# Kernel tuning notes

Hardware: AMD Instinct MI355X
Metric: run time of the kernel (lower is better)

Reference implementation:

```python
import jax, jax.numpy as jnp
import numpy as np

B, L, D = 4, 4096, 1024
H, W = 16, 64          # n_heads, window_size
HD = D // H            # head_dim
EPS = 1e-5


def setup_inputs() -> dict:
    key = jax.random.key(0)
    ks = jax.random.split(key, 3)
    s = 1.0 / np.sqrt(D)
    x = jax.random.normal(ks[0], (B, L, D), dtype=jnp.float32)
    Wqkv = (jax.random.normal(ks[1], (3 * D, D), dtype=jnp.float32) * s)
    bqkv = jnp.zeros((3 * D,), dtype=jnp.float32)
    Wproj = (jax.random.normal(ks[2], (D, D), dtype=jnp.float32) * s)
    bproj = jnp.zeros((D,), dtype=jnp.float32)
    gamma = jnp.ones((D,), dtype=jnp.float32)
    beta = jnp.zeros((D,), dtype=jnp.float32)
    return {"x": x, "Wqkv": Wqkv, "bqkv": bqkv, "Wproj": Wproj,
            "bproj": bproj, "gamma": gamma, "beta": beta}


def reference(x, Wqkv, bqkv, Wproj, bproj, gamma, beta):
    scale = HD ** -0.5
    nw = L // W  # L is a multiple of W, so pad_len == 0 (same math as padded path)
    # QKV projection -> [3, B, H, L, HD]
    qkv = (x @ Wqkv.T + bqkv).reshape(B, L, 3, H, HD).transpose(2, 0, 3, 1, 4)
    q, k, v = qkv[0], qkv[1], qkv[2]
    # split into non-overlapping windows: [B, H, nw, W, HD]
    q = q.reshape(B, H, nw, W, HD)
    k = k.reshape(B, H, nw, W, HD)
    v = v.reshape(B, H, nw, W, HD)
    attn = jax.nn.softmax(jnp.einsum('bhnqd,bhnkd->bhnqk', q, k) * scale, axis=-1)
    out = jnp.einsum('bhnqk,bhnkd->bhnqd', attn, v)  # dropout is identity in eval
    out = out.reshape(B, H, L, HD).transpose(0, 2, 1, 3).reshape(B, L, D)
    out = out @ Wproj.T + bproj
    y = out + x
    mean = jnp.mean(y, axis=-1, keepdims=True)
    var = jnp.mean((y - mean) ** 2, axis=-1, keepdims=True)
    return (y - mean) * jax.lax.rsqrt(var + EPS) * gamma + beta
```

## Files before the change

### kernel.cpp

```cpp
#include <hip/hip_runtime.h>
#include <stdint.h>


typedef __attribute__((ext_vector_type(8))) short short8;
typedef __attribute__((ext_vector_type(4))) float float4v;
typedef unsigned short us;

#define GAS const __attribute__((address_space(1))) void
#define LAS __attribute__((address_space(3))) void

__device__ __forceinline__ float bf2f(us u) {
  return __uint_as_float(((unsigned int)u) << 16);
}
__device__ __forceinline__ us f2bf(float f) {
  unsigned int u = __float_as_uint(f);
  unsigned int r = u + 0x7FFFu + ((u >> 16) & 1u);
  return (us)(r >> 16);
}
__device__ __forceinline__ int4 stage8(const float* p) {
  float4 a = *(const float4*)p;
  float4 b = *(const float4*)(p + 4);
  int4 r;
  us* u = (us*)&r;
  u[0] = f2bf(a.x); u[1] = f2bf(a.y); u[2] = f2bf(a.z); u[3] = f2bf(a.w);
  u[4] = f2bf(b.x); u[5] = f2bf(b.y); u[6] = f2bf(b.z); u[7] = f2bf(b.w);
  return r;
}
__device__ __forceinline__ int4 stage8(const us* p) { return *(const int4*)p; }
__device__ __forceinline__ void stc(us* p, float v) { *p = f2bf(v); }
__device__ __forceinline__ void stc(float* p, float v) { *p = v; }

__global__ __launch_bounds__(256) void cast_bf16(const float* __restrict__ src,
                                                 us* __restrict__ dst, int n8) {
  const int i = blockIdx.x * 256 + threadIdx.x;
  if (i < n8) *(int4*)(dst + (size_t)i * 8) = stage8(src + (size_t)i * 8);
}

template <int N, int K, int EPI, typename CT>
__global__ __launch_bounds__(256) void gemm_async(
    const us* __restrict__ A, const us* __restrict__ Bt,
    const float* __restrict__ bias, const float* __restrict__ resid,
    CT* __restrict__ C) {
  __shared__ __align__(16) us As[128 * 64];
  __shared__ __align__(16) us Bs[128 * 64];
  const int tid = threadIdx.x;
  const int lane = tid & 63;
  const int wave = tid >> 6;
  const int wm = wave >> 1, wn = wave & 1;
  const int lr = lane & 15, lq = lane >> 4;
  const int m0 = blockIdx.y * 128;
  const int n0 = blockIdx.x * 128;
  const int trow = tid >> 3;
  const int tcol = (((tid & 7) ^ (trow & 7)) * 8);

  float4v acc[4][4];
#pragma unroll
  for (int i = 0; i < 4; i++)
#pragma unroll
    for (int j = 0; j < 4; j++) acc[i][j] = (float4v)0.0f;

  for (int k0 = 0; k0 < K; k0 += 64) {
#pragma unroll
    for (int p = 0; p < 4; p++) {
      const us* ga = A + (size_t)(m0 + p * 32 + trow) * K + k0 + tcol;
      const us* gb = Bt + (size_t)(n0 + p * 32 + trow) * K + k0 + tcol;
      __builtin_amdgcn_global_load_lds((GAS*)ga, (LAS*)&As[(p * 256 + tid) * 8], 16, 0, 0);
      __builtin_amdgcn_global_load_lds((GAS*)gb, (LAS*)&Bs[(p * 256 + tid) * 8], 16, 0, 0);
    }
    __syncthreads();
#pragma unroll
    for (int kk8 = 0; kk8 < 2; kk8++) {
      short8 af[4], bfv[4];
#pragma unroll
      for (int mt = 0; mt < 4; mt++)
        af[mt] = *(const short8*)&As[(wm * 64 + mt * 16 + lr) * 64 +
                                     (((lq + kk8 * 4) ^ (lr & 7)) * 8)];
#pragma unroll
      for (int nt = 0; nt < 4; nt++)
        bfv[nt] = *(const short8*)&Bs[(wn * 64 + nt * 16 + lr) * 64 +
                                      (((lq + kk8 * 4) ^ (lr & 7)) * 8)];
#pragma unroll
      for (int mt = 0; mt < 4; mt++)
#pragma unroll
        for (int nt = 0; nt < 4; nt++)
          acc[mt][nt] = __builtin_amdgcn_mfma_f32_16x16x32_bf16(
              af[mt], bfv[nt], acc[mt][nt], 0, 0, 0);
    }
    __syncthreads();
  }

  float bb[4];
#pragma unroll
  for (int nt = 0; nt < 4; nt++) bb[nt] = bias[n0 + wn * 64 + nt * 16 + lr];
#pragma unroll
  for (int mt = 0; mt < 4; mt++) {
    const int rbase = m0 + wm * 64 + mt * 16 + lq * 4;
#pragma unroll
    for (int nt = 0; nt < 4; nt++) {
      const int col = n0 + wn * 64 + nt * 16 + lr;
#pragma unroll
      for (int r = 0; r < 4; r++) {
        float v = acc[mt][nt][r] + bb[nt];
        size_t idx = (size_t)(rbase + r) * N + col;
        if (EPI) v += resid[idx];
        stc(&C[idx], v);
      }
    }
  }
}

__global__ __launch_bounds__(256) void attn_mfma(
    const us* __restrict__ qkv, us* __restrict__ attn) {
  __shared__ __align__(16) us Vt[64 * 64];
  __shared__ __align__(16) us Pl[4 * 16 * 64];
  const int wid = blockIdx.x;
  const int wi = wid & 63;
  const int h = (wid >> 6) & 15;
  const int b = wid >> 10;
  const int tid = threadIdx.x;
  const int lane = tid & 63;
  const int w = tid >> 6;
  const int lr = lane & 15, lq = lane >> 4;
  const int rowbase = b * 4096 + wi * 64;

  {
    const int r = lane;
    const int cs = w * 16;
    const us* vsrc = qkv + (size_t)(rowbase + r) * 3072 + 2048 + h * 64 + cs;
    int4 v0 = *(const int4*)vsrc;
    int4 v1 = *(const int4*)(vsrc + 8);
    const us* vv0 = (const us*)&v0;
    const us* vv1 = (const us*)&v1;
#pragma unroll
    for (int i = 0; i < 8; i++) {
      const int d = cs + i;
      Vt[d * 64 + (((r >> 3) ^ (d & 7)) * 8) + (r & 7)] = vv0[i];
    }
#pragma unroll
    for (int i = 0; i < 8; i++) {
      const int d = cs + 8 + i;
      Vt[d * 64 + (((r >> 3) ^ (d & 7)) * 8) + (r & 7)] = vv1[i];
    }
  }

  short8 aq[2];
  {
    const us* qrow = qkv + (size_t)(rowbase + w * 16 + lr) * 3072 + h * 64 + lq * 8;
    aq[0] = *(const short8*)qrow;
    aq[1] = *(const short8*)(qrow + 32);
  }
  float4v s[4];
#pragma unroll
  for (int nt = 0; nt < 4; nt++) s[nt] = (float4v)0.0f;
#pragma unroll
  for (int kk8 = 0; kk8 < 2; kk8++) {
#pragma unroll
    for (int nt = 0; nt < 4; nt++) {
      const us* krow = qkv + (size_t)(rowbase + nt * 16 + lr) * 3072 + 1024 +
                       h * 64 + kk8 * 32 + lq * 8;
      short8 bk = *(const short8*)krow;
      s[nt] = __builtin_amdgcn_mfma_f32_16x16x32_bf16(aq[kk8], bk, s[nt], 0, 0, 0);
    }
  }

  float p[4][4];
#pragma unroll
  for (int r = 0; r < 4; r++) {
    float mx = -1e30f;
#pragma unroll
    for (int nt = 0; nt < 4; nt++) {
      s[nt][r] *= 0.125f;
      mx = fmaxf(mx, s[nt][r]);
    }
    mx = fmaxf(mx, __shfl_xor(mx, 1));
    mx = fmaxf(mx, __shfl_xor(mx, 2));
    mx = fmaxf(mx, __shfl_xor(mx, 4));
    mx = fmaxf(mx, __shfl_xor(mx, 8));
    float sum = 0.f;
#pragma unroll
    for (int nt = 0; nt < 4; nt++) {
      p[nt][r] = __expf(s[nt][r] - mx);
      sum += p[nt][r];
    }
    sum += __shfl_xor(sum, 1);
    sum += __shfl_xor(sum, 2);
    sum += __shfl_xor(sum, 4);
    sum += __shfl_xor(sum, 8);
    const float inv = 1.0f / sum;
#pragma unroll
    for (int nt = 0; nt < 4; nt++) p[nt][r] *= inv;
  }

  us* pw = Pl + w * 1024;
#pragma unroll
  for (int nt = 0; nt < 4; nt++) {
    const int c = nt * 16 + lr;
#pragma unroll
    for (int r = 0; r < 4; r++) {
      const int row = lq * 4 + r;
      pw[row * 64 + (((c >> 3) ^ (row & 7)) * 8) + (c & 7)] = f2bf(p[nt][r]);
    }
  }
  __syncthreads();

  float4v o[4];
#pragma unroll
  for (int nt = 0; nt < 4; nt++) o[nt] = (float4v)0.0f;
#pragma unroll
  for (int kk8 = 0; kk8 < 2; kk8++) {
    short8 pa = *(const short8*)&pw[lr * 64 + (((lq + kk8 * 4) ^ (lr & 7)) * 8)];
#pragma unroll
    for (int nt = 0; nt < 4; nt++) {
      const int d = nt * 16 + lr;
      short8 vb = *(const short8*)&Vt[d * 64 + (((lq + kk8 * 4) ^ (d & 7)) * 8)];
      o[nt] = __builtin_amdgcn_mfma_f32_16x16x32_bf16(pa, vb, o[nt], 0, 0, 0);
    }
  }

#pragma unroll
  for (int nt = 0; nt < 4; nt++) {
    const int d = nt * 16 + lr;
#pragma unroll
    for (int r = 0; r < 4; r++) {
      const int tok = rowbase + w * 16 + lq * 4 + r;
      attn[(size_t)tok * 1024 + h * 64 + d] = f2bf(o[nt][r]);
    }
  }
}

template <int N, int K, int EPI, typename AT, typename CT>
__global__ __launch_bounds__(256) void gemm_bt(
    const AT* __restrict__ A, const float* __restrict__ Bt,
    const float* __restrict__ bias, const float* __restrict__ resid,
    CT* __restrict__ C) {
  __shared__ __align__(16) us As[128 * 64];
  __shared__ __align__(16) us Bs[128 * 64];
  const int tid = threadIdx.x;
  const int lane = tid & 63;
  const int wave = tid >> 6;
  const int wm = wave >> 1, wn = wave & 1;
  const int lr = lane & 15, lq = lane >> 4;
  const int m0 = blockIdx.y * 128;
  const int n0 = blockIdx.x * 128;
  const int trow = tid >> 3;
  const int tcol = (tid & 7) * 8;

  float4v acc[4][4];
#pragma unroll
  for (int i = 0; i < 4; i++)
#pragma unroll
    for (int j = 0; j < 4; j++) acc[i][j] = (float4v)0.0f;

  for (int k0 = 0; k0 < K; k0 += 64) {
    int4 av[4], bv[4];
#pragma unroll
    for (int p = 0; p < 4; p++) {
      av[p] = stage8(A + (size_t)(m0 + p * 32 + trow) * K + k0 + tcol);
      bv[p] = stage8(Bt + (size_t)(n0 + p * 32 + trow) * K + k0 + tcol);
    }
#pragma unroll
    for (int p = 0; p < 4; p++) {
      *(int4*)&As[(p * 256 + tid) * 8] = av[p];
      *(int4*)&Bs[(p * 256 + tid) * 8] = bv[p];
    }
    __syncthreads();
#pragma unroll
    for (int kk = 0; kk < 64; kk += 32) {
      short8 af[4], bfv[4];
#pragma unroll
      for (int mt = 0; mt < 4; mt++)
        af[mt] = *(const short8*)&As[(wm * 64 + mt * 16 + lr) * 64 + kk + lq * 8];
#pragma unroll
      for (int nt = 0; nt < 4; nt++)
        bfv[nt] = *(const short8*)&Bs[(wn * 64 + nt * 16 + lr) * 64 + kk + lq * 8];
#pragma unroll
      for (int mt = 0; mt < 4; mt++)
#pragma unroll
        for (int nt = 0; nt < 4; nt++)
          acc[mt][nt] = __builtin_amdgcn_mfma_f32_16x16x32_bf16(
              af[mt], bfv[nt], acc[mt][nt], 0, 0, 0);
    }
    __syncthreads();
  }

  float bb[4];
#pragma unroll
  for (int nt = 0; nt < 4; nt++) bb[nt] = bias[n0 + wn * 64 + nt * 16 + lr];
#pragma unroll
  for (int mt = 0; mt < 4; mt++) {
    const int rbase = m0 + wm * 64 + mt * 16 + lq * 4;
#pragma unroll
    for (int nt = 0; nt < 4; nt++) {
      const int col = n0 + wn * 64 + nt * 16 + lr;
#pragma unroll
      for (int r = 0; r < 4; r++) {
        float v = acc[mt][nt][r] + bb[nt];
        size_t idx = (size_t)(rbase + r) * N + col;
        if (EPI) v += resid[idx];
        stc(&C[idx], v);
      }
    }
  }
}

__global__ __launch_bounds__(256) void attn_win(
    const us* __restrict__ qkv, us* __restrict__ attn) {
  __shared__ float qs[64][65];
  __shared__ float ks[64][65];
  __shared__ float vs[64][65];
  const int wid = blockIdx.x;
  const int wi = wid & 63;
  const int h = (wid >> 6) & 15;
  const int b = wid >> 10;
  const int t = threadIdx.x;
  const int rowbase = b * 4096 + wi * 64;
  {
    const int r = t >> 2;
    const int cs = (t & 3) * 16;
    const us* base = qkv + (size_t)(rowbase + r) * 3072 + h * 64 + cs;
#pragma unroll
    for (int s = 0; s < 3; s++) {
      float* dst = (s == 0) ? &qs[r][cs] : (s == 1) ? &ks[r][cs] : &vs[r][cs];
      const us* src = base + s * 1024;
#pragma unroll
      for (int half = 0; half < 2; half++) {
        int4 dv = *(const int4*)(src + half * 8);
        const us* tp = (const us*)&dv;
#pragma unroll
        for (int i = 0; i < 8; i++) dst[half * 8 + i] = bf2f(tp[i]);
      }
    }
  }
  __syncthreads();
  const int r0 = (t >> 4) * 4;
  const int c0 = (t & 15) * 4;
  float acc[4][4] = {};
#pragma unroll 8
  for (int k = 0; k < 64; k++) {
    float qv[4], kv[4];
#pragma unroll
    for (int i = 0; i < 4; i++) qv[i] = qs[r0 + i][k];
#pragma unroll
    for (int j = 0; j < 4; j++) kv[j] = ks[c0 + j][k];
#pragma unroll
    for (int i = 0; i < 4; i++)
#pragma unroll
      for (int j = 0; j < 4; j++) acc[i][j] += qv[i] * kv[j];
  }
  __syncthreads();
#pragma unroll
  for (int i = 0; i < 4; i++)
#pragma unroll
    for (int j = 0; j < 4; j++) qs[r0 + i][c0 + j] = acc[i][j] * 0.125f;
  __syncthreads();
  {
    const int rr = t >> 2;
    const int cs = (t & 3) * 16;
    float pv[16];
    float m = -1e30f;
#pragma unroll
    for (int i = 0; i < 16; i++) {
      pv[i] = qs[rr][cs + i];
      m = fmaxf(m, pv[i]);
    }
    m = fmaxf(m, __shfl_xor(m, 1));
    m = fmaxf(m, __shfl_xor(m, 2));
    float ssum = 0.f;
#pragma unroll
    for (int i = 0; i < 16; i++) {
      pv[i] = __expf(pv[i] - m);
      ssum += pv[i];
    }
    ssum += __shfl_xor(ssum, 1);
    ssum += __shfl_xor(ssum, 2);
    const float inv = 1.0f / ssum;
#pragma unroll
    for (int i = 0; i < 16; i++) qs[rr][cs + i] = pv[i] * inv;
  }
  __syncthreads();
  float o[4][4] = {};
#pragma unroll 8
  for (int k = 0; k < 64; k++) {
    float pr[4], vv[4];
#pragma unroll
    for (int i = 0; i < 4; i++) pr[i] = qs[r0 + i][k];
#pragma unroll
    for (int j = 0; j < 4; j++) vv[j] = vs[k][c0 + j];
#pragma unroll
    for (int i = 0; i < 4; i++)
#pragma unroll
      for (int j = 0; j < 4; j++) o[i][j] += pr[i] * vv[j];
  }
#pragma unroll
  for (int i = 0; i < 4; i++)
#pragma unroll
    for (int j = 0; j < 4; j++)
      attn[(size_t)(rowbase + r0 + i) * 1024 + h * 64 + c0 + j] = f2bf(o[i][j]);
}

__global__ __launch_bounds__(256) void ln_inplace(
    float* __restrict__ y, const float* __restrict__ gamma,
    const float* __restrict__ beta) {
  const int row = blockIdx.x;
  const int t = threadIdx.x;
  float* yr = y + (size_t)row * 1024;
  float4 v = *(const float4*)(yr + t * 4);
  float s1 = v.x + v.y + v.z + v.w;
  float s2 = v.x * v.x + v.y * v.y + v.z * v.z + v.w * v.w;
#pragma unroll
  for (int off = 32; off > 0; off >>= 1) {
    s1 += __shfl_down(s1, off);
    s2 += __shfl_down(s2, off);
  }
  __shared__ float red[8];
  const int lane = t & 63, wave = t >> 6;
  if (lane == 0) {
    red[wave] = s1;
    red[4 + wave] = s2;
  }
  __syncthreads();
  if (t == 0) {
    red[0] = red[0] + red[1] + red[2] + red[3];
    red[4] = red[4] + red[5] + red[6] + red[7];
  }
  __syncthreads();
  const float mean = red[0] * (1.0f / 1024.0f);
  const float var = red[4] * (1.0f / 1024.0f) - mean * mean;
  const float rstd = rsqrtf(var + 1e-5f);
  float4 g = *(const float4*)(gamma + t * 4);
  float4 bt = *(const float4*)(beta + t * 4);
  float4 o;
  o.x = (v.x - mean) * rstd * g.x + bt.x;
  o.y = (v.y - mean) * rstd * g.y + bt.y;
  o.z = (v.z - mean) * rstd * g.z + bt.z;
  o.w = (v.w - mean) * rstd * g.w + bt.w;
  *(float4*)(yr + t * 4) = o;
}

extern "C" void kernel_launch(void* const* d_in, const int* in_sizes, int n_in,
                              void* d_out, int out_size, void* d_ws,
                              size_t ws_size, hipStream_t stream) {
  const float* x = (const float*)d_in[0];
  const float* Wqkv = (const float*)d_in[1];
  const float* bqkv = (const float*)d_in[2];
  const float* Wproj = (const float*)d_in[3];
  const float* bproj = (const float*)d_in[4];
  const float* gamma = (const float*)d_in[5];
  const float* beta = (const float*)d_in[6];
  float* out = (float*)d_out;

  us* qkv = (us*)d_ws;
  us* attn = qkv + (size_t)16384 * 3072;
  us* xb = attn + (size_t)16384 * 1024;
  us* Wqkvb = xb + (size_t)16384 * 1024;
  us* Wprojb = Wqkvb + (size_t)3072 * 1024;
  const size_t need =
      ((size_t)16384 * 3072 + 3 * (size_t)16384 * 1024 + (size_t)3072 * 1024 +
       (size_t)1024 * 1024) * sizeof(us);

  if (ws_size >= need) {
    cast_bf16<<<(16384 * 1024 / 8 + 255) / 256, 256, 0, stream>>>(x, xb,
                                                                  16384 * 128);
    cast_bf16<<<(3072 * 1024 / 8 + 255) / 256, 256, 0, stream>>>(Wqkv, Wqkvb,
                                                                 3072 * 128);
    cast_bf16<<<(1024 * 1024 / 8 + 255) / 256, 256, 0, stream>>>(Wproj, Wprojb,
                                                                 1024 * 128);
    gemm_async<3072, 1024, 0, us><<<dim3(24, 128), 256, 0, stream>>>(
        xb, Wqkvb, bqkv, nullptr, qkv);
    attn_mfma<<<4096, 256, 0, stream>>>(qkv, attn);
    gemm_async<1024, 1024, 1, float><<<dim3(8, 128), 256, 0, stream>>>(
        attn, Wprojb, bproj, x, out);
  } else {
    gemm_bt<3072, 1024, 0, float, us><<<dim3(24, 128), 256, 0, stream>>>(
        x, Wqkv, bqkv, nullptr, qkv);
    attn_win<<<4096, 256, 0, stream>>>(qkv, attn);
    gemm_bt<1024, 1024, 1, us, float><<<dim3(8, 128), 256, 0, stream>>>(
        attn, Wproj, bproj, x, out);
  }
  ln_inplace<<<16384, 256, 0, stream>>>(out, gamma, beta);
}
```

Measured before the change: 385.4 us.

## Use 256x256 double-buffered GEMM tiles with async LDS prefetch and priority hints

Replaces the 128x128 single-buffered bf16 GEMM with a 256x256 tile over 512 threads. The next K-tile is double-buffered via global_load_lds and a partial vmcnt wait, so loads overlap the MFMA work. Barriers around each MFMA cluster and s_setprio raise MFMA issue priority. The larger tile improves operand reuse but uses 128KB of LDS and more accumulator registers, and launches fewer blocks, which hurts occupancy and tail balance, especially for the 1024-wide projection (256 blocks).

```diff
diff --git a/kernel.cpp b/kernel.cpp
--- a/kernel.cpp
+++ b/kernel.cpp
@@ -37,76 +37,111 @@
 }
 
 template <int N, int K, int EPI, typename CT>
-__global__ __launch_bounds__(256) void gemm_async(
+__global__ __launch_bounds__(512, 1) void gemm256(
     const us* __restrict__ A, const us* __restrict__ Bt,
     const float* __restrict__ bias, const float* __restrict__ resid,
     CT* __restrict__ C) {
-  __shared__ __align__(16) us As[128 * 64];
-  __shared__ __align__(16) us Bs[128 * 64];
+  __shared__ __align__(16) us As[2][256 * 64];
+  __shared__ __align__(16) us Bs[2][256 * 64];
   const int tid = threadIdx.x;
   const int lane = tid & 63;
   const int wave = tid >> 6;
-  const int wm = wave >> 1, wn = wave & 1;
+  const int wm = wave >> 2;
+  const int wn = wave & 3;
   const int lr = lane & 15, lq = lane >> 4;
-  const int m0 = blockIdx.y * 128;
-  const int n0 = blockIdx.x * 128;
+  const int m0 = blockIdx.y * 256;
+  const int n0 = blockIdx.x * 256;
   const int trow = tid >> 3;
   const int tcol = (((tid & 7) ^ (trow & 7)) * 8);
 
-  float4v acc[4][4];
-#pragma unroll
-  for (int i = 0; i < 4; i++)
+  constexpr int NT = K / 64;
+
+  float4v acc[8][4];
+#pragma unroll
+  for (int i = 0; i < 8; i++)
 #pragma unroll
     for (int j = 0; j < 4; j++) acc[i][j] = (float4v)0.0f;
 
-  for (int k0 = 0; k0 < K; k0 += 64) {
-#pragma unroll
-    for (int p = 0; p < 4; p++) {
-      const us* ga = A + (size_t)(m0 + p * 32 + trow) * K + k0 + tcol;
-      const us* gb = Bt + (size_t)(n0 + p * 32 + trow) * K + k0 + tcol;
-      __builtin_amdgcn_global_load_lds((GAS*)ga, (LAS*)&As[(p * 256 + tid) * 8], 16, 0, 0);
-      __builtin_amdgcn_global_load_lds((GAS*)gb, (LAS*)&Bs[(p * 256 + tid) * 8], 16, 0, 0);
-    }
-    __syncthreads();
+#define STAGE256(buf, t)                                                       \
+  do {                                                                         \
+    const size_t kof = (size_t)(t) * 64;                                       \
+    _Pragma("unroll") for (int q = 0; q < 4; q++) {                            \
+      const us* ga = A + (size_t)(m0 + q * 64 + trow) * K + kof + tcol;        \
+      __builtin_amdgcn_global_load_lds((GAS*)ga,                               \
+          (LAS*)&As[buf][(q * 512 + tid) * 8], 16, 0, 0);                      \
+    }                                                                          \
+    _Pragma("unroll") for (int q = 0; q < 4; q++) {                            \
+      const us* gb = Bt + (size_t)(n0 + q * 64 + trow) * K + kof + tcol;       \
+      __builtin_amdgcn_global_load_lds((GAS*)gb,                               \
+          (LAS*)&Bs[buf][(q * 512 + tid) * 8], 16, 0, 0);                      \
+    }                                                                          \
+  } while (0)
+
+  STAGE256(0, 0);
+
+  for (int t = 0; t < NT; t++) {
+    const int cur = t & 1;
+    if (t + 1 < NT) {
+      STAGE256(cur ^ 1, t + 1);
+      asm volatile("s_waitcnt vmcnt(8)" ::: "memory");
+    } else {
+      asm volatile("s_waitcnt vmcnt(0)" ::: "memory");
+    }
+    __builtin_amdgcn_s_barrier();
+
+    const us* Ab = As[cur];
+    const us* Bb = Bs[cur];
 #pragma unroll
     for (int kk8 = 0; kk8 < 2; kk8++) {
-      short8 af[4], bfv[4];
-#pragma unroll
-      for (int mt = 0; mt < 4; mt++)
-        af[mt] = *(const short8*)&As[(wm * 64 + mt * 16 + lr) * 64 +
-                                     (((lq + kk8 * 4) ^ (lr & 7)) * 8)];
-#pragma unroll
-      for (int nt = 0; nt < 4; nt++)
-        bfv[nt] = *(const short8*)&Bs[(wn * 64 + nt * 16 + lr) * 64 +
-                                      (((lq + kk8 * 4) ^ (lr & 7)) * 8)];
-#pragma unroll
-      for (int mt = 0; mt < 4; mt++)
-#pragma unroll
-        for (int nt = 0; nt < 4; nt++)
-          acc[mt][nt] = __builtin_amdgcn_mfma_f32_16x16x32_bf16(
-              af[mt], bfv[nt], acc[mt][nt], 0, 0, 0);
-    }
-    __syncthreads();
-  }
+      short8 bf8[4];
+#pragma unroll
+      for (int nt = 0; nt < 4; nt++) {
+        const int row = wn * 64 + nt * 16 + lr;
+        bf8[nt] = *(const short8*)&Bb[row * 64 + (((kk8 * 4 + lq) ^ (lr & 7)) * 8)];
+      }
+#pragma unroll
+      for (int mh = 0; mh < 2; mh++) {
+        short8 af[4];
+#pragma unroll
+        for (int mt = 0; mt < 4; mt++) {
+          const int row = wm * 128 + mh * 64 + mt * 16 + lr;
+          af[mt] = *(const short8*)&Ab[row * 64 + (((kk8 * 4 + lq) ^ (lr & 7)) * 8)];
+        }
+        __builtin_amdgcn_s_barrier();
+        __builtin_amdgcn_s_setprio(1);
+#pragma unroll
+        for (int mt = 0; mt < 4; mt++)
+#pragma unroll
+          for (int nt = 0; nt < 4; nt++)
+            acc[mh * 4 + mt][nt] = __builtin_amdgcn_mfma_f32_16x16x32_bf16(
+                af[mt], bf8[nt], acc[mh * 4 + mt][nt], 0, 0, 0);
+        __builtin_amdgcn_s_setprio(0);
+        __builtin_amdgcn_s_barrier();
+      }
+    }
+  }
+#undef STAGE256
 
   float bb[4];
 #pragma unroll
   for (int nt = 0; nt < 4; nt++) bb[nt] = bias[n0 + wn * 64 + nt * 16 + lr];
 #pragma unroll
-  for (int mt = 0; mt < 4; mt++) {
-    const int rbase = m0 + wm * 64 + mt * 16 + lq * 4;
-#pragma unroll
-    for (int nt = 0; nt < 4; nt++) {
-      const int col = n0 + wn * 64 + nt * 16 + lr;
-#pragma unroll
-      for (int r = 0; r < 4; r++) {
-        float v = acc[mt][nt][r] + bb[nt];
-        size_t idx = (size_t)(rbase + r) * N + col;
-        if (EPI) v += resid[idx];
-        stc(&C[idx], v);
+  for (int mh = 0; mh < 2; mh++)
+#pragma unroll
+    for (int mt = 0; mt < 4; mt++) {
+      const int rbase = m0 + wm * 128 + mh * 64 + mt * 16 + lq * 4;
+#pragma unroll
+      for (int nt = 0; nt < 4; nt++) {
+        const int col = n0 + wn * 64 + nt * 16 + lr;
+#pragma unroll
+        for (int r = 0; r < 4; r++) {
+          float v = acc[mh * 4 + mt][nt][r] + bb[nt];
+          size_t idx = (size_t)(rbase + r) * N + col;
+          if (EPI) v += resid[idx];
+          stc(&C[idx], v);
+        }
       }
     }
-  }
 }
 
 __global__ __launch_bounds__(256) void attn_mfma(
@@ -465,10 +500,10 @@
                                                                  3072 * 128);
     cast_bf16<<<(1024 * 1024 / 8 + 255) / 256, 256, 0, stream>>>(Wproj, Wprojb,
                                                                  1024 * 128);
-    gemm_async<3072, 1024, 0, us><<<dim3(24, 128), 256, 0, stream>>>(
+    gemm256<3072, 1024, 0, us><<<dim3(12, 64), 512, 0, stream>>>(
         xb, Wqkvb, bqkv, nullptr, qkv);
     attn_mfma<<<4096, 256, 0, stream>>>(qkv, attn);
-    gemm_async<1024, 1024, 1, float><<<dim3(8, 128), 256, 0, stream>>>(
+    gemm256<1024, 1024, 1, float><<<dim3(4, 64), 512, 0, stream>>>(
         attn, Wprojb, bproj, x, out);
   } else {
     gemm_bt<3072, 1024, 0, float, us><<<dim3(24, 128), 256, 0, stream>>>(
```

New measurement: 380.4 us. About the same (-1.3%).
